# Optimization experiments

Measured on AMD Instinct MI355X. Metric: run time of the kernel, lower is better.

Reference implementation:

```python
import jax, jax.numpy as jnp
import numpy as np

N = 10000
E = 320000

def leaky(x):
    return jnp.where(x >= 0, x, 0.01 * x)

def spmm(rows, cols, vals, dense):
    # sparse(N,N) @ dense(N,D) via gather + segment-sum
    return jax.ops.segment_sum(vals[:, None] * dense[cols], rows, num_segments=N)

def setup_inputs() -> dict:
    key = jax.random.key(0)
    ks = jax.random.split(key, 16)
    def xav(k, shp):
        std = float(np.sqrt(2.0 / (shp[0] + shp[1])))
        return jax.random.normal(k, shp, dtype=jnp.float32) * std
    return {
        "x": jax.random.normal(ks[0], (N, 512), dtype=jnp.float32),
        "adj_rows": jax.random.randint(ks[1], (E,), 0, N, dtype=jnp.int32),
        "adj_cols": jax.random.randint(ks[2], (E,), 0, N, dtype=jnp.int32),
        "adj_vals": jax.random.uniform(ks[3], (E,), dtype=jnp.float32),
        "W1": xav(ks[4], (512, 256)), "b1": jnp.zeros((256,), jnp.float32),
        "Wc1a": xav(ks[5], (256, 128)), "bc1a": jnp.zeros((128,), jnp.float32),
        "Wc1b": xav(ks[6], (128, 64)), "bc1b": jnp.zeros((64,), jnp.float32),
        "Wc2a": xav(ks[7], (64, 128)), "bc2a": jnp.zeros((128,), jnp.float32),
        "Wc2b": xav(ks[8], (128, 256)), "bc2b": jnp.zeros((256,), jnp.float32),
        "W6": xav(ks[9], (256, 512)), "b6": jnp.zeros((512,), jnp.float32),
    }

def reference(x, adj_rows, adj_cols, adj_vals, W1, b1, Wc1a, bc1a, Wc1b, bc1b,
              Wc2a, bc2a, Wc2b, bc2b, W6, b6):
    # encode (eval mode: dropout is identity)
    h = spmm(adj_rows, adj_cols, adj_vals, x @ W1) + b1   # gc1
    h = leaky(h)
    z = leaky(h @ Wc1a + bc1a) @ Wc1b + bc1b              # classifier1, [N,64]
    # inner-product decoder with identity activation -> dense NxN adjacency
    A = z @ z.T                                            # [N,N]
    # decode: classifier2 then gc6 applied with the DENSE reconstructed adj
    h2 = leaky(z @ Wc2a + bc2a) @ Wc2b + bc2b              # [N,256]
    h2 = leaky(h2)
    out = A @ (h2 @ W6) + b6                               # [N,512]
    return (out, z)
```

## Files before the change

### kernel.cpp

```cpp
#include <hip/hip_runtime.h>
#include <hip/hip_bf16.h>

#define NROWS 10000
#define KPAD  10240

typedef __attribute__((ext_vector_type(8))) short bf16x8;
typedef __attribute__((ext_vector_type(4))) float f32x4;

__device__ __forceinline__ float leaky_f(float x) { return x >= 0.f ? x : 0.01f * x; }

__device__ __forceinline__ unsigned short f2bf(float f) {
    union { float f; unsigned int u; } v; v.f = f;
    unsigned int r = v.u + 0x7fffu + ((v.u >> 16) & 1u);
    return (unsigned short)(r >> 16);
}
__device__ __forceinline__ float bf2f(unsigned short h) {
    union { unsigned int u; float f; } v; v.u = ((unsigned int)h) << 16;
    return v.f;
}

__global__ void conv_all(const float* __restrict__ x, const float* __restrict__ W1,
                         const float* __restrict__ Wc1a, const float* __restrict__ Wc1b,
                         const float* __restrict__ Wc2a, const float* __restrict__ Wc2b,
                         const float* __restrict__ W6,
                         unsigned short* __restrict__ XHI,
                         unsigned short* __restrict__ o1, unsigned short* __restrict__ o2,
                         unsigned short* __restrict__ o3, unsigned short* __restrict__ o4,
                         unsigned short* __restrict__ o5, unsigned short* __restrict__ o6,
                         int* __restrict__ counts, unsigned short* __restrict__ Zt,
                         unsigned short* __restrict__ H2t) {
    int gid = blockIdx.x * 256 + threadIdx.x;
    if (gid < 1280000) {
        float4 v = ((const float4*)x)[gid];
        ushort4 h;
        h.x = f2bf(v.x); h.y = f2bf(v.y); h.z = f2bf(v.z); h.w = f2bf(v.w);
        ((ushort4*)XHI)[gid] = h;
    } else if (gid < 1411072) {
        int i = gid - 1280000, k = i >> 8, n = i & 255;
        o1[n * 512 + k] = f2bf(W1[i]);
    } else if (gid < 1443840) {
        int i = gid - 1411072, k = i >> 7, n = i & 127;
        o2[n * 256 + k] = f2bf(Wc1a[i]);
    } else if (gid < 1452032) {
        int i = gid - 1443840, k = i >> 6, n = i & 63;
        o3[n * 128 + k] = f2bf(Wc1b[i]);
    } else if (gid < 1460224) {
        int i = gid - 1452032, k = i >> 7, n = i & 127;
        o4[n * 64 + k] = f2bf(Wc2a[i]);
    } else if (gid < 1492992) {
        int i = gid - 1460224, k = i >> 8, n = i & 255;
        o5[n * 128 + k] = f2bf(Wc2b[i]);
    } else if (gid < 1624064) {
        int i = gid - 1492992, k = i >> 9, n = i & 511;
        o6[n * 256 + k] = f2bf(W6[i]);
    } else if (gid < 1634064) {
        counts[gid - 1624064] = 0;
    } else if (gid < 1649424) {
        int i = gid - 1634064;
        Zt[(size_t)(i / 240) * KPAD + 10000 + (i % 240)] = 0;
    } else if (gid < 1710864) {
        int i = gid - 1649424;
        H2t[(size_t)(i / 240) * KPAD + 10000 + (i % 240)] = 0;
    }
}

__global__ void hist_kernel(const int* __restrict__ rows, int* __restrict__ counts, int E) {
    int i = blockIdx.x * blockDim.x + threadIdx.x;
    if (i < E) atomicAdd(&counts[rows[i]], 1);
}

__global__ __launch_bounds__(1024)
void scan_kernel(const int* __restrict__ counts, int* __restrict__ starts,
                 int* __restrict__ cursor, int n) {
    __shared__ int buf[1024];
    int tid = threadIdx.x;
    int base = tid * 10;
    int v[10];
    int local = 0;
#pragma unroll
    for (int j = 0; j < 10; ++j) {
        int i = base + j;
        v[j] = (i < n) ? counts[i] : 0;
        local += v[j];
    }
    buf[tid] = local;
    __syncthreads();
    for (int off = 1; off < 1024; off <<= 1) {
        int t = (tid >= off) ? buf[tid - off] : 0;
        __syncthreads();
        buf[tid] += t;
        __syncthreads();
    }
    int run = buf[tid] - local;
#pragma unroll
    for (int j = 0; j < 10; ++j) {
        int i = base + j;
        if (i < n) { starts[i] = run; cursor[i] = run; run += v[j]; }
    }
    if (tid == 1023) starts[n] = buf[1023];
}

__global__ void scatter_kernel(const int* __restrict__ rows, const int* __restrict__ cols,
                               const float* __restrict__ vals, int* __restrict__ cursor,
                               int* __restrict__ cols_s, float* __restrict__ vals_s, int E) {
    int i = blockIdx.x * blockDim.x + threadIdx.x;
    if (i < E) {
        int pos = atomicAdd(&cursor[rows[i]], 1);
        cols_s[pos] = cols[i];
        vals_s[pos] = vals[i];
    }
}

__global__ __launch_bounds__(64)
void spmm_leaky_kernel(const int* __restrict__ starts, const int* __restrict__ cols_s,
                       const float* __restrict__ vals_s, const unsigned short* __restrict__ C1b,
                       const float* __restrict__ b1, unsigned short* __restrict__ Hb) {
    int r = blockIdx.x;
    int t = threadIdx.x;
    float4 a0 = ((const float4*)b1)[t];
    float4 a1 = {0.f, 0.f, 0.f, 0.f};
    float4 a2 = {0.f, 0.f, 0.f, 0.f};
    float4 a3 = {0.f, 0.f, 0.f, 0.f};
    int s = starts[r], e = starts[r + 1];
    int p = s;
    for (; p + 4 <= e; p += 4) {
        int c0 = cols_s[p], c1 = cols_s[p + 1], c2 = cols_s[p + 2], c3 = cols_s[p + 3];
        float v0 = vals_s[p], v1 = vals_s[p + 1], v2 = vals_s[p + 2], v3 = vals_s[p + 3];
        ushort4 s0 = ((const ushort4*)(C1b + (size_t)c0 * 256))[t];
        ushort4 s1 = ((const ushort4*)(C1b + (size_t)c1 * 256))[t];
        ushort4 s2 = ((const ushort4*)(C1b + (size_t)c2 * 256))[t];
        ushort4 s3 = ((const ushort4*)(C1b + (size_t)c3 * 256))[t];
        a0.x += v0 * bf2f(s0.x); a0.y += v0 * bf2f(s0.y);
        a0.z += v0 * bf2f(s0.z); a0.w += v0 * bf2f(s0.w);
        a1.x += v1 * bf2f(s1.x); a1.y += v1 * bf2f(s1.y);
        a1.z += v1 * bf2f(s1.z); a1.w += v1 * bf2f(s1.w);
        a2.x += v2 * bf2f(s2.x); a2.y += v2 * bf2f(s2.y);
        a2.z += v2 * bf2f(s2.z); a2.w += v2 * bf2f(s2.w);
        a3.x += v3 * bf2f(s3.x); a3.y += v3 * bf2f(s3.y);
        a3.z += v3 * bf2f(s3.z); a3.w += v3 * bf2f(s3.w);
    }
    for (; p < e; ++p) {
        int c0 = cols_s[p];
        float v0 = vals_s[p];
        ushort4 s0 = ((const ushort4*)(C1b + (size_t)c0 * 256))[t];
        a0.x += v0 * bf2f(s0.x); a0.y += v0 * bf2f(s0.y);
        a0.z += v0 * bf2f(s0.z); a0.w += v0 * bf2f(s0.w);
    }
    ushort4 h;
    h.x = f2bf(leaky_f(a0.x + a1.x + a2.x + a3.x));
    h.y = f2bf(leaky_f(a0.y + a1.y + a2.y + a3.y));
    h.z = f2bf(leaky_f(a0.z + a1.z + a2.z + a3.z));
    h.w = f2bf(leaky_f(a0.w + a1.w + a2.w + a3.w));
    ((ushort4*)Hb)[(size_t)r * 64 + t] = h;
}

template<int ACT, int WF32, int WBF, int WTB>
__global__ __launch_bounds__(256)
void gemm_mfma(const unsigned short* __restrict__ A, const unsigned short* __restrict__ Bt,
               const float* __restrict__ bias, float* __restrict__ Cf,
               unsigned short* __restrict__ Cb, unsigned short* __restrict__ Ct,
               int ldt, int M, int N, int K) {
    __shared__ short sA[64][72];
    __shared__ short sB[64][72];
    const int bm = blockIdx.x * 64;
    const int bn = blockIdx.y * 64;
    const int tid = threadIdx.x;
    const int lane = tid & 63, wid = tid >> 6;
    const int wm = wid & 1, wn = wid >> 1;
    const int l15 = lane & 15, kg = lane >> 4;

    f32x4 acc[2][2];
#pragma unroll
    for (int i = 0; i < 2; i++)
#pragma unroll
        for (int j = 0; j < 2; j++) acc[i][j] = (f32x4){0.f, 0.f, 0.f, 0.f};

    for (int k0 = 0; k0 < K; k0 += 64) {
#pragma unroll
        for (int it = 0; it < 2; ++it) {
            int idx = tid + it * 256;
            int r = idx >> 3, s = idx & 7;
            int gm = bm + r;
            uint4 va = {0u, 0u, 0u, 0u};
            if (gm < M) va = *(const uint4*)(A + (size_t)gm * K + k0 + s * 8);
            *(uint4*)(&sA[r][s * 8]) = va;
            uint4 vb = *(const uint4*)(Bt + (size_t)(bn + r) * K + k0 + s * 8);
            *(uint4*)(&sB[r][s * 8]) = vb;
        }
        __syncthreads();
        bf16x8 a[2][2], b[2][2];
#pragma unroll
        for (int i = 0; i < 2; i++)
#pragma unroll
            for (int ks = 0; ks < 2; ++ks) {
                a[i][ks] = *(const bf16x8*)(&sA[wm * 32 + i * 16 + l15][kg * 8 + ks * 32]);
                b[i][ks] = *(const bf16x8*)(&sB[wn * 32 + i * 16 + l15][kg * 8 + ks * 32]);
            }
#pragma unroll
        for (int ks = 0; ks < 2; ++ks)
#pragma unroll
            for (int i = 0; i < 2; i++)
#pragma unroll
                for (int j = 0; j < 2; j++)
                    acc[i][j] = __builtin_amdgcn_mfma_f32_16x16x32_bf16(a[i][ks], b[j][ks], acc[i][j], 0, 0, 0);
        __syncthreads();
    }

#pragma unroll
    for (int i = 0; i < 2; i++) {
        int row0 = wm * 32 + i * 16 + kg * 4;
#pragma unroll
        for (int j = 0; j < 2; j++) {
            int col = bn + wn * 32 + j * 16 + l15;
            float bv = bias ? bias[col] : 0.f;
            ushort4 tw;
#pragma unroll
            for (int r = 0; r < 4; r++) {
                int grow = bm + row0 + r;
                float v = acc[i][j][r] + bv;
                if (ACT) v = leaky_f(v);
                if (WF32) { if (grow < M) Cf[(size_t)grow * N + col] = v; }
                if (WBF)  { if (grow < M) Cb[(size_t)grow * N + col] = f2bf(v); }
                if (WTB)  ((unsigned short*)&tw)[r] = f2bf(v);
            }
            if (WTB && (bm + row0) < M)
                *(ushort4*)(&Ct[(size_t)col * ldt + bm + row0]) = tw;
        }
    }
}

__global__ __launch_bounds__(256)
void fused_enc(const unsigned short* __restrict__ H,
               const unsigned short* __restrict__ Wa,
               const unsigned short* __restrict__ Wb,
               const float* __restrict__ ba, const float* __restrict__ bb,
               float* __restrict__ Zf, unsigned short* __restrict__ Zb,
               unsigned short* __restrict__ Zt, int M) {
    __shared__ short sA[64][72];
    __shared__ short sB[128][72];
    __shared__ short sT1[64][136];
    __shared__ short sWb[64][136];
    const int bm = blockIdx.x * 64;
    const int tid = threadIdx.x;
    const int lane = tid & 63, wid = tid >> 6;
    const int wm = wid & 1, wn = wid >> 1;
    const int l15 = lane & 15, kg = lane >> 4;

#pragma unroll
    for (int it = 0; it < 4; ++it) {
        int idx = tid + it * 256;
        int r = idx >> 4, s = idx & 15;
        *(uint4*)(&sWb[r][s * 8]) = *(const uint4*)(Wb + r * 128 + s * 8);
    }

    f32x4 accA[2][4];
#pragma unroll
    for (int i = 0; i < 2; i++)
#pragma unroll
        for (int j = 0; j < 4; j++) accA[i][j] = (f32x4){0.f, 0.f, 0.f, 0.f};

    for (int k0 = 0; k0 < 256; k0 += 64) {
#pragma unroll
        for (int it = 0; it < 2; ++it) {
            int idx = tid + it * 256;
            int r = idx >> 3, s = idx & 7;
            int gm = bm + r;
            uint4 va = {0u, 0u, 0u, 0u};
            if (gm < M) va = *(const uint4*)(H + (size_t)gm * 256 + k0 + s * 8);
            *(uint4*)(&sA[r][s * 8]) = va;
        }
#pragma unroll
        for (int it = 0; it < 4; ++it) {
            int idx = tid + it * 256;
            int r = idx >> 3, s = idx & 7;
            *(uint4*)(&sB[r][s * 8]) = *(const uint4*)(Wa + r * 256 + k0 + s * 8);
        }
        __syncthreads();
#pragma unroll
        for (int ks = 0; ks < 2; ++ks) {
            bf16x8 a[2], b[4];
#pragma unroll
            for (int i = 0; i < 2; i++)
                a[i] = *(const bf16x8*)(&sA[wm * 32 + i * 16 + l15][kg * 8 + ks * 32]);
#pragma unroll
            for (int j = 0; j < 4; j++)
                b[j] = *(const bf16x8*)(&sB[wn * 64 + j * 16 + l15][kg * 8 + ks * 32]);
#pragma unroll
            for (int i = 0; i < 2; i++)
#pragma unroll
                for (int j = 0; j < 4; j++)
                    accA[i][j] = __builtin_amdgcn_mfma_f32_16x16x32_bf16(a[i], b[j], accA[i][j], 0, 0, 0);
        }
        __syncthreads();
    }
#pragma unroll
    for (int i = 0; i < 2; i++) {
        int row0 = wm * 32 + i * 16 + kg * 4;
#pragma unroll
        for (int j = 0; j < 4; j++) {
            int col = wn * 64 + j * 16 + l15;
            float bv = ba[col];
#pragma unroll
            for (int r = 0; r < 4; r++)
                sT1[row0 + r][col] = f2bf(leaky_f(accA[i][j][r] + bv));
        }
    }
    __syncthreads();

    f32x4 accB[2][2];
#pragma unroll
    for (int i = 0; i < 2; i++)
#pragma unroll
        for (int j = 0; j < 2; j++) accB[i][j] = (f32x4){0.f, 0.f, 0.f, 0.f};
#pragma unroll
    for (int kc = 0; kc < 4; ++kc) {
        bf16x8 a[2], b[2];
#pragma unroll
        for (int i = 0; i < 2; i++)
            a[i] = *(const bf16x8*)(&sT1[wm * 32 + i * 16 + l15][kc * 32 + kg * 8]);
#pragma unroll
        for (int j = 0; j < 2; j++)
            b[j] = *(const bf16x8*)(&sWb[wn * 32 + j * 16 + l15][kc * 32 + kg * 8]);
#pragma unroll
        for (int i = 0; i < 2; i++)
#pragma unroll
            for (int j = 0; j < 2; j++)
                accB[i][j] = __builtin_amdgcn_mfma_f32_16x16x32_bf16(a[i], b[j], accB[i][j], 0, 0, 0);
    }
#pragma unroll
    for (int i = 0; i < 2; i++) {
        int row0 = wm * 32 + i * 16 + kg * 4;
#pragma unroll
        for (int j = 0; j < 2; j++) {
            int col = wn * 32 + j * 16 + l15;
            float bv = bb[col];
            ushort4 tw;
#pragma unroll
            for (int r = 0; r < 4; r++) {
                int grow = bm + row0 + r;
                float v = accB[i][j][r] + bv;
                if (grow < M) {
                    Zf[(size_t)grow * 64 + col] = v;
                    Zb[(size_t)grow * 64 + col] = f2bf(v);
                }
                ((unsigned short*)&tw)[r] = f2bf(v);
            }
            if ((bm + row0) < M)
                *(ushort4*)(&Zt[(size_t)col * KPAD + bm + row0]) = tw;
        }
    }
}

__global__ __launch_bounds__(256)
void fused_dec(const unsigned short* __restrict__ Z,
               const unsigned short* __restrict__ Wa,
               const unsigned short* __restrict__ Wb,
               const float* __restrict__ ba, const float* __restrict__ bb,
               unsigned short* __restrict__ H2t, int M) {
    __shared__ short sA[64][72];
    __shared__ short sB[128][72];
    __shared__ short sT2[64][136];
    __shared__ short sB2[256][72];
    const int bm = blockIdx.x * 64;
    const int tid = threadIdx.x;
    const int lane = tid & 63, wid = tid >> 6;
    const int wm = wid & 1, wn = wid >> 1;
    const int l15 = lane & 15, kg = lane >> 4;

#pragma unroll
    for (int it = 0; it < 2; ++it) {
        int idx = tid + it * 256;
        int r = idx >> 3, s = idx & 7;
        int gm = bm + r;
        uint4 va = {0u, 0u, 0u, 0u};
        if (gm < M) va = *(const uint4*)(Z + (size_t)gm * 64 + s * 8);
        *(uint4*)(&sA[r][s * 8]) = va;
    }
#pragma unroll
    for (int it = 0; it < 4; ++it) {
        int idx = tid + it * 256;
        int r = idx >> 3, s = idx & 7;
        *(uint4*)(&sB[r][s * 8]) = *(const uint4*)(Wa + r * 64 + s * 8);
    }
    __syncthreads();
    f32x4 accA[2][4];
#pragma unroll
    for (int i = 0; i < 2; i++)
#pragma unroll
        for (int j = 0; j < 4; j++) accA[i][j] = (f32x4){0.f, 0.f, 0.f, 0.f};
#pragma unroll
    for (int ks = 0; ks < 2; ++ks) {
        bf16x8 a[2], b[4];
#pragma unroll
        for (int i = 0; i < 2; i++)
            a[i] = *(const bf16x8*)(&sA[wm * 32 + i * 16 + l15][kg * 8 + ks * 32]);
#pragma unroll
        for (int j = 0; j < 4; j++)
            b[j] = *(const bf16x8*)(&sB[wn * 64 + j * 16 + l15][kg * 8 + ks * 32]);
#pragma unroll
        for (int i = 0; i < 2; i++)
#pragma unroll
            for (int j = 0; j < 4; j++)
                accA[i][j] = __builtin_amdgcn_mfma_f32_16x16x32_bf16(a[i], b[j], accA[i][j], 0, 0, 0);
    }
    __syncthreads();
#pragma unroll
    for (int i = 0; i < 2; i++) {
        int row0 = wm * 32 + i * 16 + kg * 4;
#pragma unroll
        for (int j = 0; j < 4; j++) {
            int col = wn * 64 + j * 16 + l15;
            float bv = ba[col];
#pragma unroll
            for (int r = 0; r < 4; r++)
                sT2[row0 + r][col] = f2bf(leaky_f(accA[i][j][r] + bv));
        }
    }
    __syncthreads();

    f32x4 accB[2][8];
#pragma unroll
    for (int i = 0; i < 2; i++)
#pragma unroll
        for (int j = 0; j < 8; j++) accB[i][j] = (f32x4){0.f, 0.f, 0.f, 0.f};
    for (int k0 = 0; k0 < 128; k0 += 64) {
#pragma unroll
        for (int it = 0; it < 8; ++it) {
            int idx = tid + it * 256;
            int r = idx >> 3, s = idx & 7;
            *(uint4*)(&sB2[r][s * 8]) = *(const uint4*)(Wb + r * 128 + k0 + s * 8);
        }
        __syncthreads();
#pragma unroll
        for (int ks = 0; ks < 2; ++ks) {
            bf16x8 a[2], b[8];
#pragma unroll
            for (int i = 0; i < 2; i++)
                a[i] = *(const bf16x8*)(&sT2[wm * 32 + i * 16 + l15][k0 + ks * 32 + kg * 8]);
#pragma unroll
            for (int j = 0; j < 8; j++)
                b[j] = *(const bf16x8*)(&sB2[wn * 128 + j * 16 + l15][kg * 8 + ks * 32]);
#pragma unroll
            for (int i = 0; i < 2; i++)
#pragma unroll
                for (int j = 0; j < 8; j++)
                    accB[i][j] = __builtin_amdgcn_mfma_f32_16x16x32_bf16(a[i], b[j], accB[i][j], 0, 0, 0);
        }
        __syncthreads();
    }
#pragma unroll
    for (int i = 0; i < 2; i++) {
        int row0 = wm * 32 + i * 16 + kg * 4;
#pragma unroll
        for (int j = 0; j < 8; j++) {
            int col = wn * 128 + j * 16 + l15;
            float bv = bb[col];
            ushort4 tw;
#pragma unroll
            for (int r = 0; r < 4; r++)
                ((unsigned short*)&tw)[r] = f2bf(leaky_f(accB[i][j][r] + bv));
            if ((bm + row0) < M)
                *(ushort4*)(&H2t[(size_t)col * KPAD + bm + row0]) = tw;
        }
    }
}

__global__ __launch_bounds__(256)
void sgemm_sk(const unsigned short* __restrict__ Zt, const unsigned short* __restrict__ H2t,
              float* __restrict__ part) {
    __shared__ short sA[64][72];
    __shared__ short sB[64][72];
    const int bn = blockIdx.x * 64;
    const int kc = blockIdx.y;
    const int tid = threadIdx.x;
    const int lane = tid & 63, wid = tid >> 6;
    const int wm = wid & 1, wn = wid >> 1;
    const int l15 = lane & 15, kg = lane >> 4;

    f32x4 acc[2][2];
#pragma unroll
    for (int i = 0; i < 2; i++)
#pragma unroll
        for (int j = 0; j < 2; j++) acc[i][j] = (f32x4){0.f, 0.f, 0.f, 0.f};

    for (int kk = 0; kk < 4; ++kk) {
        int k0 = kc * 256 + kk * 64;
#pragma unroll
        for (int it = 0; it < 2; ++it) {
            int idx = tid + it * 256;
            int r = idx >> 3, s = idx & 7;
            *(uint4*)(&sA[r][s * 8]) = *(const uint4*)(Zt + (size_t)r * KPAD + k0 + s * 8);
            *(uint4*)(&sB[r][s * 8]) = *(const uint4*)(H2t + (size_t)(bn + r) * KPAD + k0 + s * 8);
        }
        __syncthreads();
        bf16x8 a[2][2], b[2][2];
#pragma unroll
        for (int i = 0; i < 2; i++)
#pragma unroll
            for (int ks = 0; ks < 2; ++ks) {
                a[i][ks] = *(const bf16x8*)(&sA[wm * 32 + i * 16 + l15][kg * 8 + ks * 32]);
                b[i][ks] = *(const bf16x8*)(&sB[wn * 32 + i * 16 + l15][kg * 8 + ks * 32]);
            }
#pragma unroll
        for (int ks = 0; ks < 2; ++ks)
#pragma unroll
            for (int i = 0; i < 2; i++)
#pragma unroll
                for (int j = 0; j < 2; j++)
                    acc[i][j] = __builtin_amdgcn_mfma_f32_16x16x32_bf16(a[i][ks], b[j][ks], acc[i][j], 0, 0, 0);
        __syncthreads();
    }
#pragma unroll
    for (int i = 0; i < 2; i++) {
        int row0 = wm * 32 + i * 16 + kg * 4;
#pragma unroll
        for (int j = 0; j < 2; j++) {
            int col = bn + wn * 32 + j * 16 + l15;
#pragma unroll
            for (int r = 0; r < 4; r++)
                part[((size_t)kc * 64 + row0 + r) * 256 + col] = acc[i][j][r];
        }
    }
}

__global__ void reduce_S2(const float* __restrict__ part, unsigned short* __restrict__ S2b) {
    int i = blockIdx.x * blockDim.x + threadIdx.x;
    if (i < 64 * 256) {
        float s = 0.f;
#pragma unroll
        for (int c = 0; c < 40; ++c) s += part[(size_t)c * (64 * 256) + i];
        S2b[i] = f2bf(s);
    }
}

extern "C" void kernel_launch(void* const* d_in, const int* in_sizes, int n_in,
                              void* d_out, int out_size, void* d_ws, size_t ws_size,
                              hipStream_t stream) {
    const float* x    = (const float*)d_in[0];
    const int*   rows = (const int*)d_in[1];
    const int*   cols = (const int*)d_in[2];
    const float* vals = (const float*)d_in[3];
    const float* W1   = (const float*)d_in[4];
    const float* b1   = (const float*)d_in[5];
    const float* Wc1a = (const float*)d_in[6];
    const float* bc1a = (const float*)d_in[7];
    const float* Wc1b = (const float*)d_in[8];
    const float* bc1b = (const float*)d_in[9];
    const float* Wc2a = (const float*)d_in[10];
    const float* bc2a = (const float*)d_in[11];
    const float* Wc2b = (const float*)d_in[12];
    const float* bc2b = (const float*)d_in[13];
    const float* W6   = (const float*)d_in[14];
    const float* b6   = (const float*)d_in[15];

    const int N = NROWS;
    const int E = in_sizes[1];

    float* ws = (float*)d_ws;
    unsigned short* XHI  = (unsigned short*)(ws + 0);
    unsigned short* C1b  = (unsigned short*)(ws + 2560000);
    unsigned short* HHI  = (unsigned short*)(ws + 3840000);
    unsigned short* ZHI  = (unsigned short*)(ws + 5120000);
    unsigned short* ZT   = (unsigned short*)(ws + 5440000);
    unsigned short* H2T  = (unsigned short*)(ws + 5767680);
    float*          PART = ws + 7078400;
    unsigned short* S2B  = (unsigned short*)(ws + 7733760);
    unsigned short* W6ST = (unsigned short*)(ws + 7741952);
    unsigned short* W1T   = (unsigned short*)(ws + 7758336);
    unsigned short* WC1AT = (unsigned short*)(ws + 7823872);
    unsigned short* WC1BT = (unsigned short*)(ws + 7840256);
    unsigned short* WC2AT = (unsigned short*)(ws + 7844352);
    unsigned short* WC2BT = (unsigned short*)(ws + 7848448);
    unsigned short* W6T   = (unsigned short*)(ws + 7864832);

    int*   counts = (int*)(ws + 7930368);
    int*   starts = counts + 10000;
    int*   cursor = starts + 10001;
    int*   cols_s = cursor + 10000;
    float* vals_s = (float*)(cols_s + 320000);

    float* Out = (float*)d_out;
    float* Zp  = (float*)d_out + 5120000;

    const int GX = (N + 63) / 64;

    conv_all<<<6683, 256, 0, stream>>>(x, W1, Wc1a, Wc1b, Wc2a, Wc2b, W6, XHI,
                                       W1T, WC1AT, WC1BT, WC2AT, WC2BT, W6T,
                                       counts, ZT, H2T);

    hist_kernel<<<(E + 255) / 256, 256, 0, stream>>>(rows, counts, E);
    scan_kernel<<<1, 1024, 0, stream>>>(counts, starts, cursor, N);
    scatter_kernel<<<(E + 255) / 256, 256, 0, stream>>>(rows, cols, vals, cursor, cols_s, vals_s, E);

    gemm_mfma<0,0,1,0><<<dim3(GX, 4), 256, 0, stream>>>(XHI, W1T, nullptr,
                                                        nullptr, C1b, nullptr, 0, N, 256, 512);
    spmm_leaky_kernel<<<N, 64, 0, stream>>>(starts, cols_s, vals_s, C1b, b1, HHI);

    fused_enc<<<GX, 256, 0, stream>>>(HHI, WC1AT, WC1BT, bc1a, bc1b, Zp, ZHI, ZT, N);

    fused_dec<<<GX, 256, 0, stream>>>(ZHI, WC2AT, WC2BT, bc2a, bc2b, H2T, N);

    sgemm_sk<<<dim3(4, 40), 256, 0, stream>>>(ZT, H2T, PART);
    reduce_S2<<<64, 256, 0, stream>>>(PART, S2B);

    gemm_mfma<0,0,0,1><<<dim3(1, 8), 256, 0, stream>>>(S2B, W6T, nullptr,
                                                       nullptr, nullptr, W6ST, 64, 64, 512, 256);

    gemm_mfma<0,1,0,0><<<dim3(GX, 8), 256, 0, stream>>>(ZHI, W6ST, b6,
                                                        Out, nullptr, nullptr, 0, N, 512, 64);
}
```

Baseline: 135.6 us.

## Fuse x fp32-to-bf16 conversion into first GEMM and retune several kernels

Drops the separate conversion pass of x to bf16 and converts fp32 tiles on the fly inside a new 128-row MFMA GEMM, which saves one full write and read of the 10000x512 activation. The SpMM now packs four rows per 256-thread block, the split-K reduction uses 80 chunks of 128 instead of 40 of 256, and the final output GEMM uses 128-row tiles. Together these reduce launch and memory traffic and raise parallelism in the split-K stage. The cost is a larger partial buffer to reduce, workspace offsets shifted to make room for it, and redundant fp32 loads and conversions across the N-tiles of the first GEMM.

```diff
diff --git a/kernel.cpp b/kernel.cpp
--- a/kernel.cpp
+++ b/kernel.cpp
@@ -19,47 +19,40 @@
     return v.f;
 }
 
-__global__ void conv_all(const float* __restrict__ x, const float* __restrict__ W1,
-                         const float* __restrict__ Wc1a, const float* __restrict__ Wc1b,
-                         const float* __restrict__ Wc2a, const float* __restrict__ Wc2b,
-                         const float* __restrict__ W6,
-                         unsigned short* __restrict__ XHI,
+__global__ void conv_all(const float* __restrict__ W1, const float* __restrict__ Wc1a,
+                         const float* __restrict__ Wc1b, const float* __restrict__ Wc2a,
+                         const float* __restrict__ Wc2b, const float* __restrict__ W6,
                          unsigned short* __restrict__ o1, unsigned short* __restrict__ o2,
                          unsigned short* __restrict__ o3, unsigned short* __restrict__ o4,
                          unsigned short* __restrict__ o5, unsigned short* __restrict__ o6,
                          int* __restrict__ counts, unsigned short* __restrict__ Zt,
                          unsigned short* __restrict__ H2t) {
     int gid = blockIdx.x * 256 + threadIdx.x;
-    if (gid < 1280000) {
-        float4 v = ((const float4*)x)[gid];
-        ushort4 h;
-        h.x = f2bf(v.x); h.y = f2bf(v.y); h.z = f2bf(v.z); h.w = f2bf(v.w);
-        ((ushort4*)XHI)[gid] = h;
-    } else if (gid < 1411072) {
-        int i = gid - 1280000, k = i >> 8, n = i & 255;
+    if (gid < 131072) {
+        int i = gid, k = i >> 8, n = i & 255;
         o1[n * 512 + k] = f2bf(W1[i]);
-    } else if (gid < 1443840) {
-        int i = gid - 1411072, k = i >> 7, n = i & 127;
+    } else if (gid < 163840) {
+        int i = gid - 131072, k = i >> 7, n = i & 127;
         o2[n * 256 + k] = f2bf(Wc1a[i]);
-    } else if (gid < 1452032) {
-        int i = gid - 1443840, k = i >> 6, n = i & 63;
+    } else if (gid < 172032) {
+        int i = gid - 163840, k = i >> 6, n = i & 63;
         o3[n * 128 + k] = f2bf(Wc1b[i]);
-    } else if (gid < 1460224) {
-        int i = gid - 1452032, k = i >> 7, n = i & 127;
+    } else if (gid < 180224) {
+        int i = gid - 172032, k = i >> 7, n = i & 127;
         o4[n * 64 + k] = f2bf(Wc2a[i]);
-    } else if (gid < 1492992) {
-        int i = gid - 1460224, k = i >> 8, n = i & 255;
+    } else if (gid < 212992) {
+        int i = gid - 180224, k = i >> 8, n = i & 255;
         o5[n * 128 + k] = f2bf(Wc2b[i]);
-    } else if (gid < 1624064) {
-        int i = gid - 1492992, k = i >> 9, n = i & 511;
+    } else if (gid < 344064) {
+        int i = gid - 212992, k = i >> 9, n = i & 511;
         o6[n * 256 + k] = f2bf(W6[i]);
-    } else if (gid < 1634064) {
-        counts[gid - 1624064] = 0;
-    } else if (gid < 1649424) {
-        int i = gid - 1634064;
+    } else if (gid < 354064) {
+        counts[gid - 344064] = 0;
+    } else if (gid < 369424) {
+        int i = gid - 354064;
         Zt[(size_t)(i / 240) * KPAD + 10000 + (i % 240)] = 0;
-    } else if (gid < 1710864) {
-        int i = gid - 1649424;
+    } else if (gid < 430864) {
+        int i = gid - 369424;
         H2t[(size_t)(i / 240) * KPAD + 10000 + (i % 240)] = 0;
     }
 }
@@ -111,12 +104,12 @@
     }
 }
 
-__global__ __launch_bounds__(64)
+__global__ __launch_bounds__(256)
 void spmm_leaky_kernel(const int* __restrict__ starts, const int* __restrict__ cols_s,
                        const float* __restrict__ vals_s, const unsigned short* __restrict__ C1b,
                        const float* __restrict__ b1, unsigned short* __restrict__ Hb) {
-    int r = blockIdx.x;
-    int t = threadIdx.x;
+    int r = blockIdx.x * 4 + (threadIdx.x >> 6);
+    int t = threadIdx.x & 63;
     float4 a0 = ((const float4*)b1)[t];
     float4 a1 = {0.f, 0.f, 0.f, 0.f};
     float4 a2 = {0.f, 0.f, 0.f, 0.f};
@@ -154,6 +147,148 @@
     ((ushort4*)Hb)[(size_t)r * 64 + t] = h;
 }
 
+__global__ __launch_bounds__(256)
+void gemm_xf32(const float* __restrict__ A, const unsigned short* __restrict__ Bt,
+               unsigned short* __restrict__ Cb, int M, int N, int K) {
+    __shared__ short sA[128][72];
+    __shared__ short sB[64][72];
+    const int bm = blockIdx.x * 128;
+    const int bn = blockIdx.y * 64;
+    const int tid = threadIdx.x;
+    const int lane = tid & 63, wid = tid >> 6;
+    const int wm = wid & 1, wn = wid >> 1;
+    const int l15 = lane & 15, kg = lane >> 4;
+
+    f32x4 acc[4][2];
+#pragma unroll
+    for (int i = 0; i < 4; i++)
+#pragma unroll
+        for (int j = 0; j < 2; j++) acc[i][j] = (f32x4){0.f, 0.f, 0.f, 0.f};
+
+    for (int k0 = 0; k0 < K; k0 += 64) {
+#pragma unroll
+        for (int it = 0; it < 4; ++it) {
+            int idx = tid + it * 256;
+            int r = idx >> 3, s = idx & 7;
+            int gm = bm + r;
+            uint4 va = {0u, 0u, 0u, 0u};
+            if (gm < M) {
+                float4 f0 = *(const float4*)(A + (size_t)gm * K + k0 + s * 8);
+                float4 f1 = *(const float4*)(A + (size_t)gm * K + k0 + s * 8 + 4);
+                va.x = (unsigned)f2bf(f0.x) | ((unsigned)f2bf(f0.y) << 16);
+                va.y = (unsigned)f2bf(f0.z) | ((unsigned)f2bf(f0.w) << 16);
+                va.z = (unsigned)f2bf(f1.x) | ((unsigned)f2bf(f1.y) << 16);
+                va.w = (unsigned)f2bf(f1.z) | ((unsigned)f2bf(f1.w) << 16);
+            }
+            *(uint4*)(&sA[r][s * 8]) = va;
+        }
+#pragma unroll
+        for (int it = 0; it < 2; ++it) {
+            int idx = tid + it * 256;
+            int r = idx >> 3, s = idx & 7;
+            *(uint4*)(&sB[r][s * 8]) = *(const uint4*)(Bt + (size_t)(bn + r) * K + k0 + s * 8);
+        }
+        __syncthreads();
+#pragma unroll
+        for (int ks = 0; ks < 2; ++ks) {
+            bf16x8 a[4], b[2];
+#pragma unroll
+            for (int i = 0; i < 4; i++)
+                a[i] = *(const bf16x8*)(&sA[wm * 64 + i * 16 + l15][kg * 8 + ks * 32]);
+#pragma unroll
+            for (int j = 0; j < 2; j++)
+                b[j] = *(const bf16x8*)(&sB[wn * 32 + j * 16 + l15][kg * 8 + ks * 32]);
+#pragma unroll
+            for (int i = 0; i < 4; i++)
+#pragma unroll
+                for (int j = 0; j < 2; j++)
+                    acc[i][j] = __builtin_amdgcn_mfma_f32_16x16x32_bf16(a[i], b[j], acc[i][j], 0, 0, 0);
+        }
+        __syncthreads();
+    }
+#pragma unroll
+    for (int i = 0; i < 4; i++) {
+        int row0 = wm * 64 + i * 16 + kg * 4;
+#pragma unroll
+        for (int j = 0; j < 2; j++) {
+            int col = bn + wn * 32 + j * 16 + l15;
+#pragma unroll
+            for (int r = 0; r < 4; r++) {
+                int grow = bm + row0 + r;
+                if (grow < M) Cb[(size_t)grow * N + col] = f2bf(acc[i][j][r]);
+            }
+        }
+    }
+}
+
+__global__ __launch_bounds__(256)
+void gemm128(const unsigned short* __restrict__ A, const unsigned short* __restrict__ Bt,
+             const float* __restrict__ bias, float* __restrict__ Cf, int M, int N, int K) {
+    __shared__ short sA[128][72];
+    __shared__ short sB[64][72];
+    const int bm = blockIdx.x * 128;
+    const int bn = blockIdx.y * 64;
+    const int tid = threadIdx.x;
+    const int lane = tid & 63, wid = tid >> 6;
+    const int wm = wid & 1, wn = wid >> 1;
+    const int l15 = lane & 15, kg = lane >> 4;
+
+    f32x4 acc[4][2];
+#pragma unroll
+    for (int i = 0; i < 4; i++)
+#pragma unroll
+        for (int j = 0; j < 2; j++) acc[i][j] = (f32x4){0.f, 0.f, 0.f, 0.f};
+
+    for (int k0 = 0; k0 < K; k0 += 64) {
+#pragma unroll
+        for (int it = 0; it < 4; ++it) {
+            int idx = tid + it * 256;
+            int r = idx >> 3, s = idx & 7;
+            int gm = bm + r;
+            uint4 va = {0u, 0u, 0u, 0u};
+            if (gm < M) va = *(const uint4*)(A + (size_t)gm * K + k0 + s * 8);
+            *(uint4*)(&sA[r][s * 8]) = va;
+        }
+#pragma unroll
+        for (int it = 0; it < 2; ++it) {
+            int idx = tid + it * 256;
+            int r = idx >> 3, s = idx & 7;
+            *(uint4*)(&sB[r][s * 8]) = *(const uint4*)(Bt + (size_t)(bn + r) * K + k0 + s * 8);
+        }
+        __syncthreads();
+#pragma unroll
+        for (int ks = 0; ks < 2; ++ks) {
+            bf16x8 a[4], b[2];
+#pragma unroll
+            for (int i = 0; i < 4; i++)
+                a[i] = *(const bf16x8*)(&sA[wm * 64 + i * 16 + l15][kg * 8 + ks * 32]);
+#pragma unroll
+            for (int j = 0; j < 2; j++)
+                b[j] = *(const bf16x8*)(&sB[wn * 32 + j * 16 + l15][kg * 8 + ks * 32]);
+#pragma unroll
+            for (int i = 0; i < 4; i++)
+#pragma unroll
+                for (int j = 0; j < 2; j++)
+                    acc[i][j] = __builtin_amdgcn_mfma_f32_16x16x32_bf16(a[i], b[j], acc[i][j], 0, 0, 0);
+        }
+        __syncthreads();
+    }
+#pragma unroll
+    for (int i = 0; i < 4; i++) {
+        int row0 = wm * 64 + i * 16 + kg * 4;
+#pragma unroll
+        for (int j = 0; j < 2; j++) {
+            int col = bn + wn * 32 + j * 16 + l15;
+            float bv = bias[col];
+#pragma unroll
+            for (int r = 0; r < 4; r++) {
+                int grow = bm + row0 + r;
+                if (grow < M) Cf[(size_t)grow * N + col] = acc[i][j][r] + bv;
+            }
+        }
+    }
+}
+
 template<int ACT, int WF32, int WBF, int WTB>
 __global__ __launch_bounds__(256)
 void gemm_mfma(const unsigned short* __restrict__ A, const unsigned short* __restrict__ Bt,
@@ -483,8 +618,8 @@
 #pragma unroll
         for (int j = 0; j < 2; j++) acc[i][j] = (f32x4){0.f, 0.f, 0.f, 0.f};
 
-    for (int kk = 0; kk < 4; ++kk) {
-        int k0 = kc * 256 + kk * 64;
+    for (int kk = 0; kk < 2; ++kk) {
+        int k0 = kc * 128 + kk * 64;
 #pragma unroll
         for (int it = 0; it < 2; ++it) {
             int idx = tid + it * 256;
@@ -528,7 +663,7 @@
     if (i < 64 * 256) {
         float s = 0.f;
 #pragma unroll
-        for (int c = 0; c < 40; ++c) s += part[(size_t)c * (64 * 256) + i];
+        for (int c = 0; c < 80; ++c) s += part[(size_t)c * (64 * 256) + i];
         S2b[i] = f2bf(s);
     }
 }
@@ -557,23 +692,22 @@
     const int E = in_sizes[1];
 
     float* ws = (float*)d_ws;
-    unsigned short* XHI  = (unsigned short*)(ws + 0);
     unsigned short* C1b  = (unsigned short*)(ws + 2560000);
     unsigned short* HHI  = (unsigned short*)(ws + 3840000);
     unsigned short* ZHI  = (unsigned short*)(ws + 5120000);
     unsigned short* ZT   = (unsigned short*)(ws + 5440000);
     unsigned short* H2T  = (unsigned short*)(ws + 5767680);
     float*          PART = ws + 7078400;
-    unsigned short* S2B  = (unsigned short*)(ws + 7733760);
-    unsigned short* W6ST = (unsigned short*)(ws + 7741952);
-    unsigned short* W1T   = (unsigned short*)(ws + 7758336);
-    unsigned short* WC1AT = (unsigned short*)(ws + 7823872);
-    unsigned short* WC1BT = (unsigned short*)(ws + 7840256);
-    unsigned short* WC2AT = (unsigned short*)(ws + 7844352);
-    unsigned short* WC2BT = (unsigned short*)(ws + 7848448);
-    unsigned short* W6T   = (unsigned short*)(ws + 7864832);
-
-    int*   counts = (int*)(ws + 7930368);
+    unsigned short* S2B  = (unsigned short*)(ws + 8389120);
+    unsigned short* W6ST = (unsigned short*)(ws + 8397312);
+    unsigned short* W1T   = (unsigned short*)(ws + 8413696);
+    unsigned short* WC1AT = (unsigned short*)(ws + 8479232);
+    unsigned short* WC1BT = (unsigned short*)(ws + 8495616);
+    unsigned short* WC2AT = (unsigned short*)(ws + 8499712);
+    unsigned short* WC2BT = (unsigned short*)(ws + 8503808);
+    unsigned short* W6T   = (unsigned short*)(ws + 8520192);
+
+    int*   counts = (int*)(ws + 8585728);
     int*   starts = counts + 10000;
     int*   cursor = starts + 10001;
     int*   cols_s = cursor + 10000;
@@ -583,8 +717,9 @@
     float* Zp  = (float*)d_out + 5120000;
 
     const int GX = (N + 63) / 64;
-
-    conv_all<<<6683, 256, 0, stream>>>(x, W1, Wc1a, Wc1b, Wc2a, Wc2b, W6, XHI,
+    const int GX128 = (N + 127) / 128;
+
+    conv_all<<<1684, 256, 0, stream>>>(W1, Wc1a, Wc1b, Wc2a, Wc2b, W6,
                                        W1T, WC1AT, WC1BT, WC2AT, WC2BT, W6T,
                                        counts, ZT, H2T);
 
@@ -592,20 +727,19 @@
     scan_kernel<<<1, 1024, 0, stream>>>(counts, starts, cursor, N);
     scatter_kernel<<<(E + 255) / 256, 256, 0, stream>>>(rows, cols, vals, cursor, cols_s, vals_s, E);
 
-    gemm_mfma<0,0,1,0><<<dim3(GX, 4), 256, 0, stream>>>(XHI, W1T, nullptr,
-                                                        nullptr, C1b, nullptr, 0, N, 256, 512);
-    spmm_leaky_kernel<<<N, 64, 0, stream>>>(starts, cols_s, vals_s, C1b, b1, HHI);
+    gemm_xf32<<<dim3(GX128, 4), 256, 0, stream>>>(x, W1T, C1b, N, 256, 512);
+
+    spmm_leaky_kernel<<<N / 4, 256, 0, stream>>>(starts, cols_s, vals_s, C1b, b1, HHI);
 
     fused_enc<<<GX, 256, 0, stream>>>(HHI, WC1AT, WC1BT, bc1a, bc1b, Zp, ZHI, ZT, N);
 
     fused_dec<<<GX, 256, 0, stream>>>(ZHI, WC2AT, WC2BT, bc2a, bc2b, H2T, N);
 
-    sgemm_sk<<<dim3(4, 40), 256, 0, stream>>>(ZT, H2T, PART);
+    sgemm_sk<<<dim3(4, 80), 256, 0, stream>>>(ZT, H2T, PART);
     reduce_S2<<<64, 256, 0, stream>>>(PART, S2B);
 
     gemm_mfma<0,0,0,1><<<dim3(1, 8), 256, 0, stream>>>(S2B, W6T, nullptr,
                                                        nullptr, nullptr, W6ST, 64, 64, 512, 256);
 
-    gemm_mfma<0,1,0,0><<<dim3(GX, 8), 256, 0, stream>>>(ZHI, W6ST, b6,
-                                                        Out, nullptr, nullptr, 0, N, 512, 64);
-}
+    gemm128<<<dim3(GX128, 8), 256, 0, stream>>>(ZHI, W6ST, b6, Out, N, 512, 64);
+}
```

Measured after the change: 169.5 us. +25.0%, slower.
